# Kernel tuning notes

Hardware: AMD Instinct MI355X
Metric: run time of the kernel (lower is better)

The kernel has to match this reference:

```python
import jax, jax.numpy as jnp
import numpy as np

D = 1024
H = 16
EPS = 1e-5


def setup_inputs() -> dict:
    key = jax.random.key(0)
    ks = jax.random.split(key, 6)
    B, T, d = 4, 2048, D
    s = 0.02
    return {
        "x": jax.random.normal(ks[0], (B, T, d), jnp.float32),
        "w_attn": jax.random.normal(ks[1], (d, 3 * d), jnp.float32) * s,
        "w_o": jax.random.normal(ks[2], (d, d), jnp.float32) * s,
        "ln1_g": jnp.ones((d,), jnp.float32),
        "ln1_b": jnp.zeros((d,), jnp.float32),
        "ln2_g": jnp.ones((d,), jnp.float32),
        "ln2_b": jnp.zeros((d,), jnp.float32),
        "w_fc": jax.random.normal(ks[3], (d, 4 * d), jnp.float32) * s,
        "b_fc": jnp.zeros((4 * d,), jnp.float32),
        "w_proj": jax.random.normal(ks[4], (4 * d, d), jnp.float32) * s,
        "b_proj": jnp.zeros((d,), jnp.float32),
    }


def _layernorm(x, g, b):
    mu = jnp.mean(x, axis=-1, keepdims=True)
    var = jnp.mean(jnp.square(x - mu), axis=-1, keepdims=True)
    return (x - mu) * jax.lax.rsqrt(var + EPS) * g + b


def _attention(x, w_attn, w_o):
    B, T, d = x.shape
    hd = d // H
    qkv = x @ w_attn  # [B,T,3d]
    q, k, v = jnp.split(qkv, 3, axis=-1)
    q = q.reshape(B, T, H, hd).transpose(0, 2, 1, 3)  # [B,H,T,hd]
    k = k.reshape(B, T, H, hd).transpose(0, 2, 1, 3)
    v = v.reshape(B, T, H, hd).transpose(0, 2, 1, 3)
    att = jnp.einsum("bhqd,bhkd->bhqk", q, k) * (1.0 / np.sqrt(hd))
    mask = jnp.tril(jnp.ones((T, T), bool))
    att = jnp.where(mask, att, jnp.float32(-jnp.inf))
    att = jax.nn.softmax(att, axis=-1)
    y = jnp.einsum("bhqk,bhkd->bhqd", att, v)
    y = y.transpose(0, 2, 1, 3).reshape(B, T, d)
    return y @ w_o


def reference(x, w_attn, w_o, ln1_g, ln1_b, ln2_g, ln2_b, w_fc, b_fc, w_proj, b_proj):
    x = x + _attention(_layernorm(x, ln1_g, ln1_b), w_attn, w_o)
    h = _layernorm(x, ln2_g, ln2_b)
    h = jax.nn.gelu(h @ w_fc + b_fc, approximate=True)
    return x + h @ w_proj + b_proj
```

## Files before the change

kernel.cpp:

```cpp
#include <hip/hip_runtime.h>
#include <math.h>

#define D_MODEL 1024
#define NHEAD   16
#define HDIM    64
#define SEQ     2048
#define BATCH   4
#define NROWS   (BATCH*SEQ)

using bf16x8 = __attribute__((ext_vector_type(8))) short;
using bf16x4 = __attribute__((ext_vector_type(4))) short;
using f32x4  = __attribute__((ext_vector_type(4))) float;

__device__ __forceinline__ unsigned short f2bf(float f) {
    unsigned u = __float_as_uint(f);
    u += 0x7fffu + ((u >> 16) & 1u);
    return (unsigned short)(u >> 16);
}
__device__ __forceinline__ float bf2f(unsigned short h) {
    unsigned u = ((unsigned)h) << 16;
    return __uint_as_float(u);
}

#define ASYNC_COPY16(g, l) \
    __builtin_amdgcn_global_load_lds((__attribute__((address_space(1))) const void*)(g), \
                                     (__attribute__((address_space(3))) void*)(l), 16, 0, 0)

__global__ __launch_bounds__(256) void ln_kernel(const float* __restrict__ x,
                                                 const float* __restrict__ g,
                                                 const float* __restrict__ b,
                                                 unsigned short* __restrict__ out) {
    const int row = blockIdx.x;
    const int tid = threadIdx.x;
    const float4* x4 = (const float4*)(x + (size_t)row * D_MODEL);
    float4 v = x4[tid];
    float s  = v.x + v.y + v.z + v.w;
    float sq = v.x*v.x + v.y*v.y + v.z*v.z + v.w*v.w;
    #pragma unroll
    for (int off = 32; off >= 1; off >>= 1) {
        s  += __shfl_down(s,  off, 64);
        sq += __shfl_down(sq, off, 64);
    }
    __shared__ float rs[4], rq[4];
    const int wave = tid >> 6;
    if ((tid & 63) == 0) { rs[wave] = s; rq[wave] = sq; }
    __syncthreads();
    const float tot  = rs[0] + rs[1] + rs[2] + rs[3];
    const float totq = rq[0] + rq[1] + rq[2] + rq[3];
    const float mu   = tot * (1.0f / D_MODEL);
    const float var  = totq * (1.0f / D_MODEL) - mu * mu;
    const float rstd = rsqrtf(var + 1e-5f);
    const float4 gv = ((const float4*)g)[tid];
    const float4 bv = ((const float4*)b)[tid];
    unsigned short* o = out + (size_t)row * D_MODEL + tid * 4;
    o[0] = f2bf((v.x - mu) * rstd * gv.x + bv.x);
    o[1] = f2bf((v.y - mu) * rstd * gv.y + bv.y);
    o[2] = f2bf((v.z - mu) * rstd * gv.z + bv.z);
    o[3] = f2bf((v.w - mu) * rstd * gv.w + bv.w);
}

__global__ __launch_bounds__(256) void wt_kernel(const float* __restrict__ w,
                                                 unsigned short* __restrict__ wt,
                                                 int K, int N) {
    __shared__ float tile[32][33];
    const int n0 = blockIdx.x * 32, k0 = blockIdx.y * 32;
    const int tx = threadIdx.x & 31, ty = threadIdx.x >> 5;
    #pragma unroll
    for (int j = 0; j < 4; ++j)
        tile[ty + j * 8][tx] = w[(size_t)(k0 + ty + j * 8) * N + n0 + tx];
    __syncthreads();
    #pragma unroll
    for (int j = 0; j < 4; ++j)
        wt[(size_t)(n0 + ty + j * 8) * K + k0 + tx] = f2bf(tile[tx][ty + j * 8]);
}

__global__ __launch_bounds__(256) void gemm_qkv(const unsigned short* __restrict__ A,
                                                const unsigned short* __restrict__ Bt,
                                                unsigned short* __restrict__ qk_out,
                                                unsigned short* __restrict__ vt_out) {
    const int K = 1024;
    __shared__ __align__(16) unsigned short As[128 * 32];
    __shared__ __align__(16) unsigned short Bs[128 * 32];

    const int tid  = threadIdx.x;
    const int lane = tid & 63;
    const int wave = __builtin_amdgcn_readfirstlane(tid >> 6);
    const int quad = lane >> 4, l16 = lane & 15;
    const int wm = wave >> 1, wn = wave & 1;
    const int m0 = blockIdx.x * 128, n0 = blockIdx.y * 128;

    f32x4 acc[4][4] = {};

    const int rA = tid >> 2;
    const int p  = tid & 3;
    const int cs = (p ^ ((rA >> 1) & 3)) * 8;

    const unsigned short* Ag0 = A  + (size_t)(m0 + rA) * K + cs;
    const unsigned short* Ag1 = A  + (size_t)(m0 + rA + 64) * K + cs;
    const unsigned short* Bg0 = Bt + (size_t)(n0 + rA) * K + cs;
    const unsigned short* Bg1 = Bt + (size_t)(n0 + rA + 64) * K + cs;
    unsigned short* Al0 = As + tid * 8;
    unsigned short* Al1 = As + tid * 8 + 2048;
    unsigned short* Bl0 = Bs + tid * 8;
    unsigned short* Bl1 = Bs + tid * 8 + 2048;

    const int sw = (quad ^ ((l16 >> 1) & 3)) * 8;

    for (int kb = 0; kb < K; kb += 32) {
        ASYNC_COPY16(Ag0 + kb, Al0);
        ASYNC_COPY16(Ag1 + kb, Al1);
        ASYNC_COPY16(Bg0 + kb, Bl0);
        ASYNC_COPY16(Bg1 + kb, Bl1);
        __syncthreads();

        bf16x8 a[4], b[4];
        #pragma unroll
        for (int i = 0; i < 4; ++i)
            a[i] = *(const bf16x8*)&As[(wm * 64 + i * 16 + l16) * 32 + sw];
        #pragma unroll
        for (int j = 0; j < 4; ++j)
            b[j] = *(const bf16x8*)&Bs[(wn * 64 + j * 16 + l16) * 32 + sw];
        #pragma unroll
        for (int i = 0; i < 4; ++i)
            #pragma unroll
            for (int j = 0; j < 4; ++j)
                acc[i][j] = __builtin_amdgcn_mfma_f32_16x16x32_bf16(a[i], b[j], acc[i][j], 0, 0, 0);
        __syncthreads();
    }

    if (n0 < 2048) {
        const float sc = (n0 < 1024) ? 0.125f : 1.0f;
        #pragma unroll
        for (int i = 0; i < 4; ++i)
          #pragma unroll
          for (int j = 0; j < 4; ++j)
            #pragma unroll
            for (int r = 0; r < 4; ++r) {
                const int row = m0 + wm * 64 + i * 16 + quad * 4 + r;
                const int col = n0 + wn * 64 + j * 16 + l16;
                qk_out[(size_t)row * 2048 + col] = f2bf(acc[i][j][r] * sc);
            }
    } else {
        #pragma unroll
        for (int i = 0; i < 4; ++i)
          #pragma unroll
          for (int j = 0; j < 4; ++j) {
                const int dv  = n0 - 2048 + wn * 64 + j * 16 + l16;
                const int tok = m0 + wm * 64 + i * 16 + quad * 4;
                ushort4 pk;
                pk.x = f2bf(acc[i][j][0]); pk.y = f2bf(acc[i][j][1]);
                pk.z = f2bf(acc[i][j][2]); pk.w = f2bf(acc[i][j][3]);
                *(ushort4*)(vt_out + (size_t)dv * NROWS + tok) = pk;
            }
    }
}

template<bool GELU, bool OUT_BF16, bool PARTIAL>
__global__ __launch_bounds__(256) void gemm_bt(const unsigned short* __restrict__ A,
                                               const unsigned short* __restrict__ Bt,
                                               const float* __restrict__ bias,
                                               const float* __restrict__ resid,
                                               void* __restrict__ outp,
                                               int M, int N, int K, int Kslice) {
    __shared__ __align__(16) unsigned short As[128 * 32];
    __shared__ __align__(16) unsigned short Bs[128 * 32];

    const int tid  = threadIdx.x;
    const int lane = tid & 63;
    const int wave = __builtin_amdgcn_readfirstlane(tid >> 6);
    const int quad = lane >> 4, l16 = lane & 15;
    const int wm = wave >> 1, wn = wave & 1;
    const int m0 = blockIdx.x * 128, n0 = blockIdx.y * 128;
    const int kbeg = PARTIAL ? blockIdx.z * Kslice : 0;
    const int klen = PARTIAL ? ((blockIdx.z == gridDim.z - 1) ? (K - kbeg) : Kslice)
                             : K;

    f32x4 acc[4][4] = {};

    const int rA = tid >> 2;
    const int p  = tid & 3;
    const int cs = (p ^ ((rA >> 1) & 3)) * 8;

    const unsigned short* Ag0 = A  + (size_t)(m0 + rA) * K + cs + kbeg;
    const unsigned short* Ag1 = A  + (size_t)(m0 + rA + 64) * K + cs + kbeg;
    const unsigned short* Bg0 = Bt + (size_t)(n0 + rA) * K + cs + kbeg;
    const unsigned short* Bg1 = Bt + (size_t)(n0 + rA + 64) * K + cs + kbeg;
    unsigned short* Al0 = As + tid * 8;
    unsigned short* Al1 = As + tid * 8 + 2048;
    unsigned short* Bl0 = Bs + tid * 8;
    unsigned short* Bl1 = Bs + tid * 8 + 2048;

    const int sw = (quad ^ ((l16 >> 1) & 3)) * 8;

    for (int kb = 0; kb < klen; kb += 32) {
        ASYNC_COPY16(Ag0 + kb, Al0);
        ASYNC_COPY16(Ag1 + kb, Al1);
        ASYNC_COPY16(Bg0 + kb, Bl0);
        ASYNC_COPY16(Bg1 + kb, Bl1);
        __syncthreads();

        bf16x8 a[4], b[4];
        #pragma unroll
        for (int i = 0; i < 4; ++i)
            a[i] = *(const bf16x8*)&As[(wm * 64 + i * 16 + l16) * 32 + sw];
        #pragma unroll
        for (int j = 0; j < 4; ++j)
            b[j] = *(const bf16x8*)&Bs[(wn * 64 + j * 16 + l16) * 32 + sw];
        #pragma unroll
        for (int i = 0; i < 4; ++i)
            #pragma unroll
            for (int j = 0; j < 4; ++j)
                acc[i][j] = __builtin_amdgcn_mfma_f32_16x16x32_bf16(a[i], b[j], acc[i][j], 0, 0, 0);
        __syncthreads();
    }

    unsigned short* outb = (unsigned short*)outp;
    if (PARTIAL) outb += (size_t)blockIdx.z * M * N;

    #pragma unroll
    for (int i = 0; i < 4; ++i)
      #pragma unroll
      for (int j = 0; j < 4; ++j)
        #pragma unroll
        for (int r = 0; r < 4; ++r) {
            const int row = m0 + wm * 64 + i * 16 + quad * 4 + r;
            const int col = n0 + wn * 64 + j * 16 + l16;
            float v = acc[i][j][r];
            if (PARTIAL) {
                outb[(size_t)row * N + col] = f2bf(v);
            } else {
                if (bias) v += bias[col];
                if (GELU) {
                    const float u = 0.7978845608028654f * (v + 0.044715f * v * v * v);
                    const float e = __expf(2.0f * u);
                    v = 0.5f * v * (2.0f - 2.0f / (e + 1.0f));
                }
                if (resid) v += resid[(size_t)row * N + col];
                if (OUT_BF16) outb[(size_t)row * N + col] = f2bf(v);
                else          ((float*)outp)[(size_t)row * N + col] = v;
            }
        }
}

__global__ __launch_bounds__(256, 2) void gemm_big(const unsigned short* __restrict__ A,
                                                   const unsigned short* __restrict__ Bt,
                                                   const float* __restrict__ bias,
                                                   unsigned short* __restrict__ outb,
                                                   int M, int N, int K) {
    __shared__ __align__(16) unsigned short As[256 * 32];
    __shared__ __align__(16) unsigned short Bs[128 * 32];

    const int tid  = threadIdx.x;
    const int lane = tid & 63;
    const int wave = __builtin_amdgcn_readfirstlane(tid >> 6);
    const int quad = lane >> 4, l16 = lane & 15;
    const int wm = wave >> 1, wn = wave & 1;
    const int m0 = blockIdx.x * 256, n0 = blockIdx.y * 128;

    f32x4 acc[8][4] = {};

    const int rr = tid >> 2;
    const int p  = tid & 3;
    const int cs = (p ^ ((rr >> 1) & 3)) * 8;

    const unsigned short* Ag[4];
    const unsigned short* Bg[2];
    #pragma unroll
    for (int i = 0; i < 4; ++i)
        Ag[i] = A + (size_t)(m0 + i * 64 + rr) * K + cs;
    #pragma unroll
    for (int i = 0; i < 2; ++i)
        Bg[i] = Bt + (size_t)(n0 + i * 64 + rr) * K + cs;

    const int sw = (quad ^ ((l16 >> 1) & 3)) * 8;

    for (int kb = 0; kb < K; kb += 32) {
        #pragma unroll
        for (int i = 0; i < 4; ++i)
            ASYNC_COPY16(Ag[i] + kb, As + i * 2048 + tid * 8);
        #pragma unroll
        for (int i = 0; i < 2; ++i)
            ASYNC_COPY16(Bg[i] + kb, Bs + i * 2048 + tid * 8);
        __syncthreads();

        bf16x8 b[4];
        #pragma unroll
        for (int j = 0; j < 4; ++j)
            b[j] = *(const bf16x8*)&Bs[(wn * 64 + j * 16 + l16) * 32 + sw];
        #pragma unroll
        for (int i = 0; i < 8; ++i) {
            bf16x8 a = *(const bf16x8*)&As[(wm * 128 + i * 16 + l16) * 32 + sw];
            #pragma unroll
            for (int j = 0; j < 4; ++j)
                acc[i][j] = __builtin_amdgcn_mfma_f32_16x16x32_bf16(a, b[j], acc[i][j], 0, 0, 0);
        }
        __syncthreads();
    }

    #pragma unroll
    for (int i = 0; i < 8; ++i)
      #pragma unroll
      for (int j = 0; j < 4; ++j)
        #pragma unroll
        for (int r = 0; r < 4; ++r) {
            const int row = m0 + wm * 128 + i * 16 + quad * 4 + r;
            const int col = n0 + wn * 64 + j * 16 + l16;
            float v = acc[i][j][r] + bias[col];
            const float u = 0.7978845608028654f * (v + 0.044715f * v * v * v);
            const float e = __expf(2.0f * u);
            v = 0.5f * v * (2.0f - 2.0f / (e + 1.0f));
            outb[(size_t)row * N + col] = f2bf(v);
        }
}

__global__ __launch_bounds__(256) void reduce_wo_ln2(const float* __restrict__ x,
                                                     const unsigned short* __restrict__ pw,
                                                     const float* __restrict__ g,
                                                     const float* __restrict__ bb,
                                                     float* __restrict__ out,
                                                     unsigned short* __restrict__ lnout) {
    const int row = blockIdx.x;
    const int tid = threadIdx.x;
    const size_t base = (size_t)row * D_MODEL + tid * 4;
    const size_t stride = (size_t)NROWS * D_MODEL;
    float4 v = *(const float4*)(x + base);
    #pragma unroll
    for (int z = 0; z < 4; ++z) {
        ushort4 a = *(const ushort4*)(pw + z * stride + base);
        v.x += bf2f(a.x); v.y += bf2f(a.y); v.z += bf2f(a.z); v.w += bf2f(a.w);
    }
    *(float4*)(out + base) = v;

    float s  = v.x + v.y + v.z + v.w;
    float sq = v.x*v.x + v.y*v.y + v.z*v.z + v.w*v.w;
    #pragma unroll
    for (int off = 32; off >= 1; off >>= 1) {
        s  += __shfl_down(s,  off, 64);
        sq += __shfl_down(sq, off, 64);
    }
    __shared__ float rs[4], rq[4];
    const int wave = tid >> 6;
    if ((tid & 63) == 0) { rs[wave] = s; rq[wave] = sq; }
    __syncthreads();
    const float tot  = rs[0] + rs[1] + rs[2] + rs[3];
    const float totq = rq[0] + rq[1] + rq[2] + rq[3];
    const float mu   = tot * (1.0f / D_MODEL);
    const float var  = totq * (1.0f / D_MODEL) - mu * mu;
    const float rstd = rsqrtf(var + 1e-5f);
    const float4 gv = ((const float4*)g)[tid];
    const float4 bv = ((const float4*)bb)[tid];
    unsigned short* o = lnout + (size_t)row * D_MODEL + tid * 4;
    o[0] = f2bf((v.x - mu) * rstd * gv.x + bv.x);
    o[1] = f2bf((v.y - mu) * rstd * gv.y + bv.y);
    o[2] = f2bf((v.z - mu) * rstd * gv.z + bv.z);
    o[3] = f2bf((v.w - mu) * rstd * gv.w + bv.w);
}

__global__ __launch_bounds__(256) void reduce_kernel(float* __restrict__ out,
                                                     const unsigned short* __restrict__ pp,
                                                     const float* __restrict__ bias) {
    const int row = blockIdx.x;
    const int c0 = threadIdx.x * 4;
    const size_t base = (size_t)row * D_MODEL + c0;
    const size_t stride = (size_t)NROWS * D_MODEL;
    float4 o = *(float4*)(out + base);
    const float4 bs = *(const float4*)(bias + c0);
    o.x += bs.x; o.y += bs.y; o.z += bs.z; o.w += bs.w;
    #pragma unroll
    for (int z = 0; z < 3; ++z) {
        ushort4 a = *(const ushort4*)(pp + z * stride + base);
        o.x += bf2f(a.x); o.y += bf2f(a.y); o.z += bf2f(a.z); o.w += bf2f(a.w);
    }
    *(float4*)(out + base) = o;
}

__global__ __launch_bounds__(256) void attn_kernel(const unsigned short* __restrict__ qk,
                                                   const unsigned short* __restrict__ VT,
                                                   unsigned short* __restrict__ y) {
    __shared__ __align__(16) unsigned short Qs[128 * 64];
    __shared__ __align__(16) unsigned short Ks[64 * 64];
    __shared__ __align__(16) unsigned short Vs[80 * 64];
    __shared__ __align__(16) unsigned short Ps[128 * 68];

    const int tid  = threadIdx.x;
    const int lane = tid & 63, w = tid >> 6;
    const int quad = lane >> 4, l16 = lane & 15;
    const int s7   = l16 & 7;
    const int pc0  = (quad ^ s7) * 8;
    const int pc1  = ((quad + 4) ^ s7) * 8;
    const int srow = tid >> 3, sp = tid & 7;

    const int pairidx = blockIdx.x;
    const int bh = blockIdx.y;
    const int b = bh >> 4, h = bh & 15;
    const size_t rowbase = (size_t)b * SEQ;
    const unsigned short* Qbase = qk + h * 64;
    const unsigned short* Kbase = qk + 1024 + h * 64;
    const unsigned short* Vbase = VT + (size_t)(h * 64) * NROWS + b * SEQ;

    #pragma unroll
    for (int e = 0; e < 4; ++e) {
        const int off = tid * 4 + e;
        Vs[4096 + off] = (off < 64) ? (unsigned short)0x3F80 : (unsigned short)0;
    }

    for (int phase = 0; phase < 2; ++phase) {
        const int Q = phase ? pairidx : (15 - pairidx);
        const int nkt = 2 * Q + 2;
        const int qg0 = Q * 128;

        #pragma unroll
        for (int i = 0; i < 4; ++i) {
            const int row = i * 32 + srow;
            const int c = sp ^ (row & 7);
            ASYNC_COPY16(Qbase + (rowbase + qg0 + row) * 2048 + c * 8,
                         (char*)Qs + i * 4096 + tid * 16);
        }
        __syncthreads();

        bf16x8 aq[2][2];
        #pragma unroll
        for (int sub = 0; sub < 2; ++sub) {
            const int qrow = sub * 64 + w * 16 + l16;
            aq[sub][0] = *(const bf16x8*)&Qs[qrow * 64 + pc0];
            aq[sub][1] = *(const bf16x8*)&Qs[qrow * 64 + pc1];
        }

        f32x4 o[2][5] = {};

        for (int kt = 0; kt < nkt; ++kt) {
            #pragma unroll
            for (int i = 0; i < 2; ++i) {
                const int row = i * 32 + srow;
                const int c = sp ^ (row & 7);
                ASYNC_COPY16(Kbase + (rowbase + kt * 64 + row) * 2048 + c * 8,
                             (char*)Ks + i * 4096 + tid * 16);
                ASYNC_COPY16(Vbase + (size_t)row * NROWS + kt * 64 + c * 8,
                             (char*)Vs + i * 4096 + tid * 16);
            }
            __syncthreads();

            bf16x8 bk[4][2];
            #pragma unroll
            for (int cb = 0; cb < 4; ++cb) {
                const int krow = cb * 16 + l16;
                bk[cb][0] = *(const bf16x8*)&Ks[krow * 64 + pc0];
                bk[cb][1] = *(const bf16x8*)&Ks[krow * 64 + pc1];
            }

            #pragma unroll
            for (int sub = 0; sub < 2; ++sub) {
                if (kt > 2 * Q + sub) continue;
                f32x4 s[4] = {};
                #pragma unroll
                for (int cb = 0; cb < 4; ++cb) {
                    s[cb] = __builtin_amdgcn_mfma_f32_16x16x32_bf16(aq[sub][0], bk[cb][0], s[cb], 0, 0, 0);
                    s[cb] = __builtin_amdgcn_mfma_f32_16x16x32_bf16(aq[sub][1], bk[cb][1], s[cb], 0, 0, 0);
                }
                const int prow0 = sub * 64 + w * 16 + quad * 4;
                if (kt == 2 * Q + sub) {
                    const int qg = qg0 + prow0;
                    const int kg = kt * 64 + l16;
                    #pragma unroll
                    for (int cb = 0; cb < 4; ++cb)
                        #pragma unroll
                        for (int r = 0; r < 4; ++r) {
                            const float e = __expf(s[cb][r]);
                            const float pv = (kg + cb * 16 > qg + r) ? 0.0f : e;
                            Ps[(prow0 + r) * 68 + cb * 16 + l16] = f2bf(pv);
                        }
                } else {
                    #pragma unroll
                    for (int cb = 0; cb < 4; ++cb)
                        #pragma unroll
                        for (int r = 0; r < 4; ++r)
                            Ps[(prow0 + r) * 68 + cb * 16 + l16] = f2bf(__expf(s[cb][r]));
                }
            }
            __syncthreads();

            bf16x8 bv[5][2];
            #pragma unroll
            for (int db = 0; db < 5; ++db) {
                const int vrow = db * 16 + l16;
                bv[db][0] = *(const bf16x8*)&Vs[vrow * 64 + pc0];
                bv[db][1] = *(const bf16x8*)&Vs[vrow * 64 + pc1];
            }
            #pragma unroll
            for (int sub = 0; sub < 2; ++sub) {
                if (kt > 2 * Q + sub) continue;
                const unsigned short* pb = &Ps[(sub * 64 + w * 16 + l16) * 68];
                bf16x8 ap0, ap1;
                *(bf16x4*)&ap0       = *(const bf16x4*)(pb + quad * 8);
                *((bf16x4*)&ap0 + 1) = *(const bf16x4*)(pb + quad * 8 + 4);
                *(bf16x4*)&ap1       = *(const bf16x4*)(pb + 32 + quad * 8);
                *((bf16x4*)&ap1 + 1) = *(const bf16x4*)(pb + 32 + quad * 8 + 4);
                #pragma unroll
                for (int db = 0; db < 5; ++db) {
                    o[sub][db] = __builtin_amdgcn_mfma_f32_16x16x32_bf16(ap0, bv[db][0], o[sub][db], 0, 0, 0);
                    o[sub][db] = __builtin_amdgcn_mfma_f32_16x16x32_bf16(ap1, bv[db][1], o[sub][db], 0, 0, 0);
                }
            }
            __syncthreads();
        }

        #pragma unroll
        for (int sub = 0; sub < 2; ++sub)
            #pragma unroll
            for (int r = 0; r < 4; ++r) {
                const float lsum = __shfl(o[sub][4][r], lane & 48);
                const float rinv = 1.0f / lsum;
                const int trow = qg0 + sub * 64 + w * 16 + quad * 4 + r;
                unsigned short* yp = y + (rowbase + trow) * (size_t)D_MODEL + h * 64 + l16;
                #pragma unroll
                for (int db = 0; db < 4; ++db)
                    yp[db * 16] = f2bf(o[sub][db][r] * rinv);
            }
    }
}

extern "C" void kernel_launch(void* const* d_in, const int* in_sizes, int n_in,
                              void* d_out, int out_size, void* d_ws, size_t ws_size,
                              hipStream_t stream) {
    (void)in_sizes; (void)n_in; (void)out_size; (void)ws_size;
    const float* x      = (const float*)d_in[0];
    const float* w_attn = (const float*)d_in[1];
    const float* w_o    = (const float*)d_in[2];
    const float* ln1_g  = (const float*)d_in[3];
    const float* ln1_b  = (const float*)d_in[4];
    const float* ln2_g  = (const float*)d_in[5];
    const float* ln2_b  = (const float*)d_in[6];
    const float* w_fc   = (const float*)d_in[7];
    const float* b_fc   = (const float*)d_in[8];
    const float* w_proj = (const float*)d_in[9];
    const float* b_proj = (const float*)d_in[10];
    float* out = (float*)d_out;

    char* ws = (char*)d_ws;
    const size_t MiB = 1048576;
    unsigned short* ln_buf  = (unsigned short*)ws;
    unsigned short* qkbuf   = (unsigned short*)(ws + 16 * MiB);
    unsigned short* VTbuf   = (unsigned short*)(ws + 48 * MiB);
    unsigned short* wt_attn = (unsigned short*)(ws + 64 * MiB);
    unsigned short* hbuf    = (unsigned short*)(ws + 64 * MiB);
    unsigned short* wt_o    = (unsigned short*)(ws + 126 * MiB);
    unsigned short* pw      = (unsigned short*)(ws + 16 * MiB);
    unsigned short* wt_fc   = (unsigned short*)(ws + 48 * MiB);
    unsigned short* wt_proj = (unsigned short*)(ws + 56 * MiB);
    unsigned short* pp      = (unsigned short*)ws;

    wt_kernel<<<dim3(3072 / 32, 1024 / 32), 256, 0, stream>>>(w_attn, wt_attn, 1024, 3072);
    wt_kernel<<<dim3(1024 / 32, 1024 / 32), 256, 0, stream>>>(w_o, wt_o, 1024, 1024);

    ln_kernel<<<NROWS, 256, 0, stream>>>(x, ln1_g, ln1_b, ln_buf);

    gemm_qkv<<<dim3(NROWS / 128, 3072 / 128), 256, 0, stream>>>(
        ln_buf, wt_attn, qkbuf, VTbuf);

    attn_kernel<<<dim3(8, BATCH * NHEAD), 256, 0, stream>>>(qkbuf, VTbuf, ln_buf);

    gemm_bt<false, true, true><<<dim3(NROWS / 128, 1024 / 128, 4), 256, 0, stream>>>(
        ln_buf, wt_o, nullptr, nullptr, pw, NROWS, 1024, 1024, 256);
    reduce_wo_ln2<<<NROWS, 256, 0, stream>>>(x, pw, ln2_g, ln2_b, out, ln_buf);

    wt_kernel<<<dim3(4096 / 32, 1024 / 32), 256, 0, stream>>>(w_fc, wt_fc, 1024, 4096);
    wt_kernel<<<dim3(1024 / 32, 4096 / 32), 256, 0, stream>>>(w_proj, wt_proj, 4096, 1024);

    gemm_big<<<dim3(NROWS / 256, 4096 / 128), 256, 0, stream>>>(
        ln_buf, wt_fc, b_fc, hbuf, NROWS, 4096, 1024);

    gemm_bt<false, true, true><<<dim3(NROWS / 128, 1024 / 128, 3), 256, 0, stream>>>(
        hbuf, wt_proj, nullptr, nullptr, pp, NROWS, 1024, 4096, 1344);
    reduce_kernel<<<NROWS, 256, 0, stream>>>(out, pp, b_proj);
}
```

Measured before the change: 546.3 us.

## Unify GEMMs into 256x128 tiled kernel with K=64 steps for QKV, FC, proj

```diff
diff --git a/kernel.cpp b/kernel.cpp
--- a/kernel.cpp
+++ b/kernel.cpp
@@ -74,93 +74,133 @@
         wt[(size_t)(n0 + ty + j * 8) * K + k0 + tx] = f2bf(tile[tx][ty + j * 8]);
 }
 
-__global__ __launch_bounds__(256) void gemm_qkv(const unsigned short* __restrict__ A,
-                                                const unsigned short* __restrict__ Bt,
-                                                unsigned short* __restrict__ qk_out,
-                                                unsigned short* __restrict__ vt_out) {
-    const int K = 1024;
-    __shared__ __align__(16) unsigned short As[128 * 32];
-    __shared__ __align__(16) unsigned short Bs[128 * 32];
+template<int MODE>
+__global__ __launch_bounds__(256, 2) void gemm_big(const unsigned short* __restrict__ A,
+                                                   const unsigned short* __restrict__ Bt,
+                                                   const float* __restrict__ bias,
+                                                   unsigned short* __restrict__ outp,
+                                                   unsigned short* __restrict__ vt_out,
+                                                   int M, int N, int K, int Kslice) {
+    __shared__ __align__(16) unsigned short As[256 * 64];
+    __shared__ __align__(16) unsigned short Bs[128 * 64];
 
     const int tid  = threadIdx.x;
     const int lane = tid & 63;
     const int wave = __builtin_amdgcn_readfirstlane(tid >> 6);
     const int quad = lane >> 4, l16 = lane & 15;
     const int wm = wave >> 1, wn = wave & 1;
-    const int m0 = blockIdx.x * 128, n0 = blockIdx.y * 128;
-
-    f32x4 acc[4][4] = {};
-
-    const int rA = tid >> 2;
-    const int p  = tid & 3;
-    const int cs = (p ^ ((rA >> 1) & 3)) * 8;
-
-    const unsigned short* Ag0 = A  + (size_t)(m0 + rA) * K + cs;
-    const unsigned short* Ag1 = A  + (size_t)(m0 + rA + 64) * K + cs;
-    const unsigned short* Bg0 = Bt + (size_t)(n0 + rA) * K + cs;
-    const unsigned short* Bg1 = Bt + (size_t)(n0 + rA + 64) * K + cs;
-    unsigned short* Al0 = As + tid * 8;
-    unsigned short* Al1 = As + tid * 8 + 2048;
-    unsigned short* Bl0 = Bs + tid * 8;
-    unsigned short* Bl1 = Bs + tid * 8 + 2048;
-
-    const int sw = (quad ^ ((l16 >> 1) & 3)) * 8;
-
-    for (int kb = 0; kb < K; kb += 32) {
-        ASYNC_COPY16(Ag0 + kb, Al0);
-        ASYNC_COPY16(Ag1 + kb, Al1);
-        ASYNC_COPY16(Bg0 + kb, Bl0);
-        ASYNC_COPY16(Bg1 + kb, Bl1);
+    const int m0 = blockIdx.x * 256, n0 = blockIdx.y * 128;
+
+    int kbeg = 0, klen = K;
+    if (MODE == 1) {
+        kbeg = blockIdx.z * Kslice;
+        klen = (blockIdx.z == gridDim.z - 1) ? (K - kbeg) : Kslice;
+    }
+
+    f32x4 acc[8][4] = {};
+
+    const int rr  = tid >> 3;
+    const int p   = tid & 7;
+    const int gch = (p ^ (rr & 7)) * 8;
+
+    const unsigned short* Ag[8];
+    const unsigned short* Bg[4];
+    #pragma unroll
+    for (int i = 0; i < 8; ++i)
+        Ag[i] = A + (size_t)(m0 + i * 32 + rr) * K + gch + kbeg;
+    #pragma unroll
+    for (int i = 0; i < 4; ++i)
+        Bg[i] = Bt + (size_t)(n0 + i * 32 + rr) * K + gch + kbeg;
+
+    const int pc = (quad ^ (l16 & 7)) * 8;
+
+    for (int kb = 0; kb < klen; kb += 64) {
+        #pragma unroll
+        for (int i = 0; i < 8; ++i)
+            ASYNC_COPY16(Ag[i] + kb, As + i * 2048 + tid * 8);
+        #pragma unroll
+        for (int i = 0; i < 4; ++i)
+            ASYNC_COPY16(Bg[i] + kb, Bs + i * 2048 + tid * 8);
         __syncthreads();
 
-        bf16x8 a[4], b[4];
-        #pragma unroll
-        for (int i = 0; i < 4; ++i)
-            a[i] = *(const bf16x8*)&As[(wm * 64 + i * 16 + l16) * 32 + sw];
-        #pragma unroll
-        for (int j = 0; j < 4; ++j)
-            b[j] = *(const bf16x8*)&Bs[(wn * 64 + j * 16 + l16) * 32 + sw];
-        #pragma unroll
-        for (int i = 0; i < 4; ++i)
+        #pragma unroll
+        for (int half = 0; half < 2; ++half) {
+            const int off = half ? (pc ^ 32) : pc;
+            bf16x8 b[4];
             #pragma unroll
             for (int j = 0; j < 4; ++j)
-                acc[i][j] = __builtin_amdgcn_mfma_f32_16x16x32_bf16(a[i], b[j], acc[i][j], 0, 0, 0);
+                b[j] = *(const bf16x8*)&Bs[(wn * 64 + j * 16 + l16) * 64 + off];
+            #pragma unroll
+            for (int i = 0; i < 8; ++i) {
+                bf16x8 a = *(const bf16x8*)&As[(wm * 128 + i * 16 + l16) * 64 + off];
+                #pragma unroll
+                for (int j = 0; j < 4; ++j)
+                    acc[i][j] = __builtin_amdgcn_mfma_f32_16x16x32_bf16(a, b[j], acc[i][j], 0, 0, 0);
+            }
+        }
         __syncthreads();
     }
 
-    if (n0 < 2048) {
-        const float sc = (n0 < 1024) ? 0.125f : 1.0f;
-        #pragma unroll
-        for (int i = 0; i < 4; ++i)
+    if (MODE == 0) {
+        #pragma unroll
+        for (int i = 0; i < 8; ++i)
           #pragma unroll
           for (int j = 0; j < 4; ++j)
             #pragma unroll
             for (int r = 0; r < 4; ++r) {
-                const int row = m0 + wm * 64 + i * 16 + quad * 4 + r;
+                const int row = m0 + wm * 128 + i * 16 + quad * 4 + r;
                 const int col = n0 + wn * 64 + j * 16 + l16;
-                qk_out[(size_t)row * 2048 + col] = f2bf(acc[i][j][r] * sc);
+                float v = acc[i][j][r] + bias[col];
+                const float u = 0.7978845608028654f * (v + 0.044715f * v * v * v);
+                const float e = __expf(2.0f * u);
+                v = 0.5f * v * (2.0f - 2.0f / (e + 1.0f));
+                outp[(size_t)row * N + col] = f2bf(v);
+            }
+    } else if (MODE == 1) {
+        unsigned short* outb = outp + (size_t)blockIdx.z * M * N;
+        #pragma unroll
+        for (int i = 0; i < 8; ++i)
+          #pragma unroll
+          for (int j = 0; j < 4; ++j)
+            #pragma unroll
+            for (int r = 0; r < 4; ++r) {
+                const int row = m0 + wm * 128 + i * 16 + quad * 4 + r;
+                const int col = n0 + wn * 64 + j * 16 + l16;
+                outb[(size_t)row * N + col] = f2bf(acc[i][j][r]);
             }
     } else {
-        #pragma unroll
-        for (int i = 0; i < 4; ++i)
-          #pragma unroll
-          for (int j = 0; j < 4; ++j) {
-                const int dv  = n0 - 2048 + wn * 64 + j * 16 + l16;
-                const int tok = m0 + wm * 64 + i * 16 + quad * 4;
-                ushort4 pk;
-                pk.x = f2bf(acc[i][j][0]); pk.y = f2bf(acc[i][j][1]);
-                pk.z = f2bf(acc[i][j][2]); pk.w = f2bf(acc[i][j][3]);
-                *(ushort4*)(vt_out + (size_t)dv * NROWS + tok) = pk;
-            }
-    }
-}
-
-template<bool GELU, bool OUT_BF16, bool PARTIAL>
+        if (n0 < 2048) {
+            const float sc = (n0 < 1024) ? 0.125f : 1.0f;
+            #pragma unroll
+            for (int i = 0; i < 8; ++i)
+              #pragma unroll
+              for (int j = 0; j < 4; ++j)
+                #pragma unroll
+                for (int r = 0; r < 4; ++r) {
+                    const int row = m0 + wm * 128 + i * 16 + quad * 4 + r;
+                    const int col = n0 + wn * 64 + j * 16 + l16;
+                    outp[(size_t)row * 2048 + col] = f2bf(acc[i][j][r] * sc);
+                }
+        } else {
+            #pragma unroll
+            for (int i = 0; i < 8; ++i)
+              #pragma unroll
+              for (int j = 0; j < 4; ++j) {
+                    const int dv  = n0 - 2048 + wn * 64 + j * 16 + l16;
+                    const int tok = m0 + wm * 128 + i * 16 + quad * 4;
+                    ushort4 pk;
+                    pk.x = f2bf(acc[i][j][0]); pk.y = f2bf(acc[i][j][1]);
+                    pk.z = f2bf(acc[i][j][2]); pk.w = f2bf(acc[i][j][3]);
+                    *(ushort4*)(vt_out + (size_t)dv * NROWS + tok) = pk;
+                }
+        }
+    }
+}
+
+template<bool PARTIAL>
 __global__ __launch_bounds__(256) void gemm_bt(const unsigned short* __restrict__ A,
                                                const unsigned short* __restrict__ Bt,
-                                               const float* __restrict__ bias,
-                                               const float* __restrict__ resid,
-                                               void* __restrict__ outp,
+                                               unsigned short* __restrict__ outb,
                                                int M, int N, int K, int Kslice) {
     __shared__ __align__(16) unsigned short As[128 * 32];
     __shared__ __align__(16) unsigned short Bs[128 * 32];
@@ -172,8 +212,7 @@
     const int wm = wave >> 1, wn = wave & 1;
     const int m0 = blockIdx.x * 128, n0 = blockIdx.y * 128;
     const int kbeg = PARTIAL ? blockIdx.z * Kslice : 0;
-    const int klen = PARTIAL ? ((blockIdx.z == gridDim.z - 1) ? (K - kbeg) : Kslice)
-                             : K;
+    const int klen = PARTIAL ? ((blockIdx.z == gridDim.z - 1) ? (K - kbeg) : Kslice) : K;
 
     f32x4 acc[4][4] = {};
 
@@ -214,8 +253,8 @@
         __syncthreads();
     }
 
-    unsigned short* outb = (unsigned short*)outp;
-    if (PARTIAL) outb += (size_t)blockIdx.z * M * N;
+    unsigned short* ob = outb;
+    if (PARTIAL) ob += (size_t)blockIdx.z * M * N;
 
     #pragma unroll
     for (int i = 0; i < 4; ++i)
@@ -225,91 +264,7 @@
         for (int r = 0; r < 4; ++r) {
             const int row = m0 + wm * 64 + i * 16 + quad * 4 + r;
             const int col = n0 + wn * 64 + j * 16 + l16;
-            float v = acc[i][j][r];
-            if (PARTIAL) {
-                outb[(size_t)row * N + col] = f2bf(v);
-            } else {
-                if (bias) v += bias[col];
-                if (GELU) {
-                    const float u = 0.7978845608028654f * (v + 0.044715f * v * v * v);
-                    const float e = __expf(2.0f * u);
-                    v = 0.5f * v * (2.0f - 2.0f / (e + 1.0f));
-                }
-                if (resid) v += resid[(size_t)row * N + col];
-                if (OUT_BF16) outb[(size_t)row * N + col] = f2bf(v);
-                else          ((float*)outp)[(size_t)row * N + col] = v;
-            }
-        }
-}
-
-__global__ __launch_bounds__(256, 2) void gemm_big(const unsigned short* __restrict__ A,
-                                                   const unsigned short* __restrict__ Bt,
-                                                   const float* __restrict__ bias,
-                                                   unsigned short* __restrict__ outb,
-                                                   int M, int N, int K) {
-    __shared__ __align__(16) unsigned short As[256 * 32];
-    __shared__ __align__(16) unsigned short Bs[128 * 32];
-
-    const int tid  = threadIdx.x;
-    const int lane = tid & 63;
-    const int wave = __builtin_amdgcn_readfirstlane(tid >> 6);
-    const int quad = lane >> 4, l16 = lane & 15;
-    const int wm = wave >> 1, wn = wave & 1;
-    const int m0 = blockIdx.x * 256, n0 = blockIdx.y * 128;
-
-    f32x4 acc[8][4] = {};
-
-    const int rr = tid >> 2;
-    const int p  = tid & 3;
-    const int cs = (p ^ ((rr >> 1) & 3)) * 8;
-
-    const unsigned short* Ag[4];
-    const unsigned short* Bg[2];
-    #pragma unroll
-    for (int i = 0; i < 4; ++i)
-        Ag[i] = A + (size_t)(m0 + i * 64 + rr) * K + cs;
-    #pragma unroll
-    for (int i = 0; i < 2; ++i)
-        Bg[i] = Bt + (size_t)(n0 + i * 64 + rr) * K + cs;
-
-    const int sw = (quad ^ ((l16 >> 1) & 3)) * 8;
-
-    for (int kb = 0; kb < K; kb += 32) {
-        #pragma unroll
-        for (int i = 0; i < 4; ++i)
-            ASYNC_COPY16(Ag[i] + kb, As + i * 2048 + tid * 8);
-        #pragma unroll
-        for (int i = 0; i < 2; ++i)
-            ASYNC_COPY16(Bg[i] + kb, Bs + i * 2048 + tid * 8);
-        __syncthreads();
-
-        bf16x8 b[4];
-        #pragma unroll
-        for (int j = 0; j < 4; ++j)
-            b[j] = *(const bf16x8*)&Bs[(wn * 64 + j * 16 + l16) * 32 + sw];
-        #pragma unroll
-        for (int i = 0; i < 8; ++i) {
-            bf16x8 a = *(const bf16x8*)&As[(wm * 128 + i * 16 + l16) * 32 + sw];
-            #pragma unroll
-            for (int j = 0; j < 4; ++j)
-                acc[i][j] = __builtin_amdgcn_mfma_f32_16x16x32_bf16(a, b[j], acc[i][j], 0, 0, 0);
-        }
-        __syncthreads();
-    }
-
-    #pragma unroll
-    for (int i = 0; i < 8; ++i)
-      #pragma unroll
-      for (int j = 0; j < 4; ++j)
-        #pragma unroll
-        for (int r = 0; r < 4; ++r) {
-            const int row = m0 + wm * 128 + i * 16 + quad * 4 + r;
-            const int col = n0 + wn * 64 + j * 16 + l16;
-            float v = acc[i][j][r] + bias[col];
-            const float u = 0.7978845608028654f * (v + 0.044715f * v * v * v);
-            const float e = __expf(2.0f * u);
-            v = 0.5f * v * (2.0f - 2.0f / (e + 1.0f));
-            outb[(size_t)row * N + col] = f2bf(v);
+            ob[(size_t)row * N + col] = f2bf(acc[i][j][r]);
         }
 }
 
@@ -554,22 +509,22 @@
 
     ln_kernel<<<NROWS, 256, 0, stream>>>(x, ln1_g, ln1_b, ln_buf);
 
-    gemm_qkv<<<dim3(NROWS / 128, 3072 / 128), 256, 0, stream>>>(
-        ln_buf, wt_attn, qkbuf, VTbuf);
+    gemm_big<2><<<dim3(NROWS / 256, 3072 / 128), 256, 0, stream>>>(
+        ln_buf, wt_attn, nullptr, qkbuf, VTbuf, NROWS, 3072, 1024, 0);
 
     attn_kernel<<<dim3(8, BATCH * NHEAD), 256, 0, stream>>>(qkbuf, VTbuf, ln_buf);
 
-    gemm_bt<false, true, true><<<dim3(NROWS / 128, 1024 / 128, 4), 256, 0, stream>>>(
-        ln_buf, wt_o, nullptr, nullptr, pw, NROWS, 1024, 1024, 256);
+    gemm_bt<true><<<dim3(NROWS / 128, 1024 / 128, 4), 256, 0, stream>>>(
+        ln_buf, wt_o, pw, NROWS, 1024, 1024, 256);
     reduce_wo_ln2<<<NROWS, 256, 0, stream>>>(x, pw, ln2_g, ln2_b, out, ln_buf);
 
     wt_kernel<<<dim3(4096 / 32, 1024 / 32), 256, 0, stream>>>(w_fc, wt_fc, 1024, 4096);
     wt_kernel<<<dim3(1024 / 32, 4096 / 32), 256, 0, stream>>>(w_proj, wt_proj, 4096, 1024);
 
-    gemm_big<<<dim3(NROWS / 256, 4096 / 128), 256, 0, stream>>>(
-        ln_buf, wt_fc, b_fc, hbuf, NROWS, 4096, 1024);
-
-    gemm_bt<false, true, true><<<dim3(NROWS / 128, 1024 / 128, 3), 256, 0, stream>>>(
-        hbuf, wt_proj, nullptr, nullptr, pp, NROWS, 1024, 4096, 1344);
+    gemm_big<0><<<dim3(NROWS / 256, 4096 / 128), 256, 0, stream>>>(
+        ln_buf, wt_fc, b_fc, hbuf, nullptr, NROWS, 4096, 1024, 0);
+
+    gemm_big<1><<<dim3(NROWS / 256, 1024 / 128, 3), 256, 0, stream>>>(
+        hbuf, wt_proj, nullptr, pp, nullptr, NROWS, 1024, 4096, 1344);
     reduce_kernel<<<NROWS, 256, 0, stream>>>(out, pp, b_proj);
 }
```

Result: faster. 513.9 us (-5.9%).
